# Kernel tuning notes

Hardware: AMD Instinct MI355X
Metric: run time of the kernel (lower is better)

Reference implementation:

```python
import jax, jax.numpy as jnp
import numpy as np

G = 4  # number of groups


def _group_vals(h, shift, Ua, Ua1, Ua2, Ua3):
    # h: [B, H]; Ua: [g, H/g, r]; Ua1/2/3: [g, r, H/g]
    B, H = h.shape
    hg = h.reshape(B, G, H // G)
    if shift:
        # torch index = rotate-left by `shift`: new group j reads old group (j+shift)%g
        hg = jnp.roll(hg, -shift, axis=1)
    t = jnp.einsum('bgd,gdr->bgr', hg, Ua)  # shared low-rank projection
    proj = lambda M: jnp.einsum('bgr,grd->bgd', t, M).reshape(B, H)
    return proj(Ua1), proj(Ua2), proj(Ua3)


def setup_inputs() -> dict:
    key = jax.random.key(0)
    ks = jax.random.split(key, 24)
    B, I, H, wR = 8192, 1024, 1024, 256
    hg = H // G
    r01, r23 = 64, 32
    d = {}
    d['x'] = jax.random.normal(ks[0], (B, I), dtype=jnp.float32)
    d['h'] = jax.random.normal(ks[1], (B, H), dtype=jnp.float32)
    d['W'] = 0.1 * jax.random.normal(ks[2], (I, wR), dtype=jnp.float32)
    d['W1'] = 0.1 * jax.random.normal(ks[3], (wR, H), dtype=jnp.float32)
    d['W2'] = 0.1 * jax.random.normal(ks[4], (wR, H), dtype=jnp.float32)
    d['W3'] = 0.1 * jax.random.normal(ks[5], (wR, H), dtype=jnp.float32)
    d['U'] = 0.1 * jax.random.normal(ks[6], (G, hg, r01), dtype=jnp.float32)
    d['U1'] = 0.1 * jax.random.normal(ks[7], (G, r01, hg), dtype=jnp.float32)
    d['U2'] = 0.1 * jax.random.normal(ks[8], (G, r01, hg), dtype=jnp.float32)
    d['U3'] = 0.1 * jax.random.normal(ks[9], (G, r01, hg), dtype=jnp.float32)
    d['UU'] = 0.1 * jax.random.normal(ks[10], (G, hg, r01), dtype=jnp.float32)
    d['UU1'] = 0.1 * jax.random.normal(ks[11], (G, r01, hg), dtype=jnp.float32)
    d['UU2'] = 0.1 * jax.random.normal(ks[12], (G, r01, hg), dtype=jnp.float32)
    d['UU3'] = 0.1 * jax.random.normal(ks[13], (G, r01, hg), dtype=jnp.float32)
    d['UUU'] = 0.1 * jax.random.normal(ks[14], (G, hg, r23), dtype=jnp.float32)
    d['UUU1'] = 0.1 * jax.random.normal(ks[15], (G, r23, hg), dtype=jnp.float32)
    d['UUU2'] = 0.1 * jax.random.normal(ks[16], (G, r23, hg), dtype=jnp.float32)
    d['UUU3'] = 0.1 * jax.random.normal(ks[17], (G, r23, hg), dtype=jnp.float32)
    d['UUUU'] = 0.1 * jax.random.normal(ks[18], (G, hg, r23), dtype=jnp.float32)
    d['UUUU1'] = 0.1 * jax.random.normal(ks[19], (G, r23, hg), dtype=jnp.float32)
    d['UUUU2'] = 0.1 * jax.random.normal(ks[20], (G, r23, hg), dtype=jnp.float32)
    d['UUUU3'] = 0.1 * jax.random.normal(ks[21], (G, r23, hg), dtype=jnp.float32)
    d['bias_r'] = jnp.ones((1, H), dtype=jnp.float32)
    d['bias_gate'] = jnp.ones((1, H), dtype=jnp.float32)
    d['bias_update'] = jnp.ones((1, H), dtype=jnp.float32)
    return d


def reference(x, h, W, W1, W2, W3, U, U1, U2, U3, UU, UU1, UU2, UU3,
              UUU, UUU1, UUU2, UUU3, UUUU, UUUU1, UUUU2, UUUU3,
              bias_r, bias_gate, bias_update):
    u1, u2, u3 = _group_vals(h, 0, U, U1, U2, U3)
    uu1, uu2, uu3 = _group_vals(h, 1, UU, UU1, UU2, UU3)
    uuu1, uuu2, uuu3 = _group_vals(h, 2, UUU, UUU1, UUU2, UUU3)
    uuuu1, uuuu2, uuuu3 = _group_vals(h, 3, UUUU, UUUU1, UUUU2, UUUU3)
    xw = x @ W  # [B, wRank]
    w1, w2, w3 = xw @ W1, xw @ W2, xw @ W3
    r = jax.nn.sigmoid(w1 + u1 + uu1 + uuu1 + uuuu1 + bias_r)
    z = jax.nn.sigmoid(w2 + u2 + uu2 + uuu2 + uuuu2 + bias_gate)
    c_tilda = jnp.tanh(w3 + r * (u3 + uu3 + uuu3 + uuuu3) + bias_update)
    return z * h + (1.0 - z) * c_tilda
```

## Files before the change

kernel.cpp:

```cpp
#include <hip/hip_runtime.h>

typedef short bf16x8 __attribute__((ext_vector_type(8)));
typedef float f32x4 __attribute__((ext_vector_type(4)));
typedef float f32x16 __attribute__((ext_vector_type(16)));

__device__ __forceinline__ unsigned short f2bf(float f) {
  union { float f; unsigned u; } c; c.f = f;
  unsigned u = c.u;
  u += 0x7FFFu + ((u >> 16) & 1u);
  return (unsigned short)(u >> 16);
}
__device__ __forceinline__ float bf2f(unsigned short h) {
  union { unsigned u; float f; } c; c.u = ((unsigned)h) << 16;
  return c.f;
}
__device__ __forceinline__ void split2(float v, unsigned short& hi, unsigned short& lo) {
  union { float f; unsigned u; } c; c.f = v;
  unsigned uh = c.u & 0xFFFF0000u;
  hi = (unsigned short)(uh >> 16);
  union { unsigned u; float f; } d; d.u = uh;
  lo = f2bf(v - d.f);
}
__device__ __forceinline__ void gload16(const void* g, void* l) {
  __builtin_amdgcn_global_load_lds((const __attribute__((address_space(1))) void*)g,
                                   (__attribute__((address_space(3))) void*)l, 16, 0, 0);
}
__device__ __forceinline__ float sigm(float x) { return 1.0f / (1.0f + __expf(-x)); }
__device__ __forceinline__ float tanha(float x) { return 1.0f - 2.0f / (1.0f + __expf(2.0f * x)); }

__device__ __forceinline__ size_t fragIdxA(int row, int col) {
  int mb = row >> 7, rb = (row >> 5) & 3, l5 = row & 31;
  int cc = col >> 6, k4 = (col >> 4) & 3, hi = (col >> 3) & 1, e = col & 7;
  return ((size_t)(mb * 20 + cc) * 16 + rb * 4 + k4) * 512 + (hi * 32 + l5) * 8 + e;
}

__global__ __launch_bounds__(256) void s123(
    const float* __restrict__ W,
    const float* __restrict__ U, const float* __restrict__ UU,
    const float* __restrict__ UUU, const float* __restrict__ UUUU,
    const float* __restrict__ W1, const float* __restrict__ W2, const float* __restrict__ W3,
    const float* __restrict__ A1, const float* __restrict__ A2, const float* __restrict__ A3,
    const float* __restrict__ B1, const float* __restrict__ B2, const float* __restrict__ B3,
    const float* __restrict__ C1, const float* __restrict__ C2, const float* __restrict__ C3,
    const float* __restrict__ D1, const float* __restrict__ D2, const float* __restrict__ D3,
    unsigned short* __restrict__ Wt, unsigned short* __restrict__ Bg,
    unsigned short* __restrict__ Btp) {
  int gidx = blockIdx.x * 256 + threadIdx.x;
  if (gidx < 262144) {
    int idx = gidx;
    int n = idx >> 10, k = idx & 1023;
    Wt[idx] = f2bf(W[k * 256 + n]);
  } else if (gidx < 458752) {
    int idx = gidx - 262144;
    int g = idx / 49152;
    int rem = idx - g * 49152;
    int n = rem >> 8, k = rem & 255;
    int jj = 0, rr = n;
#pragma unroll
    for (int s = 0; s < 3; ++s) {
      int w = (((g - jj) & 3) < 2) ? 64 : 32;
      if (rr >= w) { rr -= w; ++jj; }
    }
    int v = (g - jj) & 3;
    int rv = (v < 2) ? 64 : 32;
    const float* M = (v == 0) ? U : (v == 1) ? UU : (v == 2) ? UUU : UUUU;
    Bg[idx] = f2bf(M[(jj * 256 + k) * rv + rr]);
  } else {
    int idx = gidx - 458752;
    int blk = idx / 12288;
    int w   = idx - blk * 12288;
    int frag = w >> 9, fl = (w >> 3) & 63, e = w & 7;
    int cb = blk & 3, jk = blk >> 2;
    int kt = jk % 11, j = jk / 11;
    int q = frag >> 3, colblk = (frag >> 2) & 1, k4 = frag & 3;
    int c  = cb * 64 + colblk * 32 + (fl & 31);
    int k2 = k4 * 16 + (fl >> 5) * 8 + e;
    float val;
    if (kt < 8) {
      int kk = (kt * 64 + k2) & 255;
      const float* Wp = (q == 0) ? W1 : (q == 1) ? W2 : W3;
      val = Wp[kk * 1024 + j * 256 + c];
    } else {
      int kT = (kt - 8) * 64 + k2;
      int v, r, rv;
      if (kT < 64)       { v = 0; r = kT;       rv = 64; }
      else if (kT < 128) { v = 1; r = kT - 64;  rv = 64; }
      else if (kT < 160) { v = 2; r = kT - 128; rv = 32; }
      else               { v = 3; r = kT - 160; rv = 32; }
      const float* M;
      if (v == 0)      M = (q == 0) ? A1 : (q == 1) ? A2 : A3;
      else if (v == 1) M = (q == 0) ? B1 : (q == 1) ? B2 : B3;
      else if (v == 2) M = (q == 0) ? C1 : (q == 1) ? C2 : C3;
      else             M = (q == 0) ? D1 : (q == 1) ? D2 : D3;
      val = M[(j * rv + r) * 256 + c];
    }
    Btp[idx] = f2bf(val);
  }
}

__device__ __forceinline__ void g1_body(const float* __restrict__ x,
                                        const unsigned short* __restrict__ Wt,
                                        unsigned short* __restrict__ Abuf,
                                        char* lds, int mb, int nb, int tid) {
  const int lane = tid & 63, wid = tid >> 6;
  const int wm = 0, wn = wid;
  f32x4 acc[2][2] = {};
  float4 xr[2];
  const int r0 = tid >> 4, f4c = tid & 15;
  const float* xbase = x + (size_t)(mb * 32) * 1024 + f4c * 4;
  (void)wm;

  auto loadX = [&](int kt) {
#pragma unroll
    for (int q = 0; q < 2; ++q)
      xr[q] = *(const float4*)(xbase + (size_t)(q * 16 + r0) * 1024 + kt * 64);
  };
  auto writeA = [&](int buf) {
#pragma unroll
    for (int q = 0; q < 2; ++q) {
      int row = q * 16 + r0;
      float4 v = xr[q];
      unsigned short h0, h1, h2, h3, l0, l1, l2, l3;
      split2(v.x, h0, l0); split2(v.y, h1, l1);
      split2(v.z, h2, l2); split2(v.w, h3, l3);
      int ba = row * 128 + ((f4c * 8) ^ ((row & 7) << 4));
      *(uint2*)(lds + buf * 4096 + ba) =
          make_uint2(((unsigned)h1 << 16) | h0, ((unsigned)h3 << 16) | h2);
      *(uint2*)(lds + 8192 + buf * 4096 + ba) =
          make_uint2(((unsigned)l1 << 16) | l0, ((unsigned)l3 << 16) | l2);
    }
  };
  auto stageB = [&](int kt, int buf) {
#pragma unroll
    for (int it = 0; it < 4; ++it) {
      int nloc = it * 32 + wid * 8 + (lane >> 3);
      const char* src = (const char*)Wt + (size_t)(nb * 128 + nloc) * 2048 + kt * 128
                        + (((lane & 7) * 16) ^ ((nloc & 7) << 4));
      gload16(src, lds + 16384 + buf * 16384 + (it * 32 + wid * 8) * 128);
    }
  };

  loadX(0); stageB(0, 0); writeA(0);
  __syncthreads();
#pragma unroll 2
  for (int kt = 0; kt < 16; ++kt) {
    int buf = kt & 1;
    if (kt < 15) {
      loadX(kt + 1); stageB(kt + 1, buf ^ 1);
      asm volatile("s_waitcnt vmcnt(6)" ::: "memory");
    } else {
      asm volatile("s_waitcnt vmcnt(0)" ::: "memory");
    }
    __builtin_amdgcn_s_barrier();
    __builtin_amdgcn_sched_barrier(0);
    const char* hA = lds + buf * 4096;
    const char* lA = lds + 8192 + buf * 4096;
    const char* bB = lds + 16384 + buf * 16384;
#pragma unroll
    for (int ks = 0; ks < 2; ++ks) {
      bf16x8 ah[2], al[2], b[2];
#pragma unroll
      for (int mf = 0; mf < 2; ++mf) {
        int mloc = mf * 16 + (lane & 15);
        int ka = (ks * 64 + (lane >> 4) * 16) ^ ((mloc & 7) << 4);
        ah[mf] = *(const bf16x8*)(hA + mloc * 128 + ka);
        al[mf] = *(const bf16x8*)(lA + mloc * 128 + ka);
      }
#pragma unroll
      for (int nf = 0; nf < 2; ++nf) {
        int nloc = wn * 32 + nf * 16 + (lane & 15);
        int kb = (ks * 64 + (lane >> 4) * 16) ^ ((nloc & 7) << 4);
        b[nf] = *(const bf16x8*)(bB + nloc * 128 + kb);
      }
#pragma unroll
      for (int mf = 0; mf < 2; ++mf)
#pragma unroll
        for (int nf = 0; nf < 2; ++nf) {
          acc[mf][nf] = __builtin_amdgcn_mfma_f32_16x16x32_bf16(ah[mf], b[nf], acc[mf][nf], 0, 0, 0);
          acc[mf][nf] = __builtin_amdgcn_mfma_f32_16x16x32_bf16(al[mf], b[nf], acc[mf][nf], 0, 0, 0);
        }
    }
    if (kt < 15) writeA(buf ^ 1);
    __builtin_amdgcn_sched_barrier(0);
    asm volatile("s_waitcnt lgkmcnt(0)" ::: "memory");
    __builtin_amdgcn_s_barrier();
  }
#pragma unroll
  for (int mf = 0; mf < 2; ++mf)
#pragma unroll
    for (int nf = 0; nf < 2; ++nf)
#pragma unroll
      for (int r = 0; r < 4; ++r) {
        int row = mb * 32 + mf * 16 + (lane >> 4) * 4 + r;
        int col = nb * 128 + wn * 32 + nf * 16 + (lane & 15);
        float val = acc[mf][nf][r];
        unsigned short hi, lo;
        split2(val, hi, lo);
        Abuf[fragIdxA(row, col)] = hi;
        Abuf[fragIdxA(row, col + 256)] = lo;
      }
}

__device__ __forceinline__ void g2_body(const float* __restrict__ h,
                                        const unsigned short* __restrict__ Bg,
                                        unsigned short* __restrict__ Abuf,
                                        char* lds, int mb, int g, int tid) {
  const int lane = tid & 63, wid = tid >> 6;
  const int wm = wid >> 1, wn = wid & 1;
  f32x4 acc[2][6] = {};
  float4 hr[4];
  const int r0 = tid >> 4, f4c = tid & 15;
  const float* hbase = h + (size_t)(mb * 64) * 1024 + g * 256 + f4c * 4;

  auto loadH = [&](int kt) {
#pragma unroll
    for (int q = 0; q < 4; ++q)
      hr[q] = *(const float4*)(hbase + (size_t)(q * 16 + r0) * 1024 + kt * 64);
  };
  auto writeA = [&](int buf) {
#pragma unroll
    for (int q = 0; q < 4; ++q) {
      int row = q * 16 + r0;
      float4 v = hr[q];
      int ba = row * 128 + ((f4c * 8) ^ ((row & 7) << 4));
      *(uint2*)(lds + buf * 8192 + ba) =
          make_uint2(((unsigned)f2bf(v.y) << 16) | f2bf(v.x),
                     ((unsigned)f2bf(v.w) << 16) | f2bf(v.z));
    }
  };
  auto stageB = [&](int kt, int buf) {
#pragma unroll
    for (int it = 0; it < 6; ++it) {
      int nloc = it * 32 + wid * 8 + (lane >> 3);
      const char* src = (const char*)Bg + (size_t)(g * 192 + nloc) * 512 + kt * 128
                        + (((lane & 7) * 16) ^ ((nloc & 7) << 4));
      gload16(src, lds + 16384 + buf * 24576 + (it * 32 + wid * 8) * 128);
    }
  };

  loadH(0); stageB(0, 0); writeA(0);
  __syncthreads();
#pragma unroll
  for (int kt = 0; kt < 4; ++kt) {
    int buf = kt & 1;
    if (kt < 3) { loadH(kt + 1); stageB(kt + 1, buf ^ 1); }
    const char* cA = lds + buf * 8192;
    const char* cB = lds + 16384 + buf * 24576;
#pragma unroll
    for (int ks = 0; ks < 2; ++ks) {
      bf16x8 a[2], b[6];
#pragma unroll
      for (int mf = 0; mf < 2; ++mf) {
        int mloc = wm * 32 + mf * 16 + (lane & 15);
        int ka = (ks * 64 + (lane >> 4) * 16) ^ ((mloc & 7) << 4);
        a[mf] = *(const bf16x8*)(cA + mloc * 128 + ka);
      }
#pragma unroll
      for (int nf = 0; nf < 6; ++nf) {
        int nloc = wn * 96 + nf * 16 + (lane & 15);
        int kb = (ks * 64 + (lane >> 4) * 16) ^ ((nloc & 7) << 4);
        b[nf] = *(const bf16x8*)(cB + nloc * 128 + kb);
      }
#pragma unroll
      for (int mf = 0; mf < 2; ++mf)
#pragma unroll
        for (int nf = 0; nf < 6; ++nf)
          acc[mf][nf] = __builtin_amdgcn_mfma_f32_16x16x32_bf16(a[mf], b[nf], acc[mf][nf], 0, 0, 0);
    }
    if (kt < 3) writeA(buf ^ 1);
    __syncthreads();
  }
#pragma unroll
  for (int mf = 0; mf < 2; ++mf)
#pragma unroll
    for (int nf = 0; nf < 6; ++nf) {
      int n = wn * 96 + nf * 16 + (lane & 15);
      int jj = 0, rr = n;
#pragma unroll
      for (int s = 0; s < 3; ++s) {
        int w = (((g - jj) & 3) < 2) ? 64 : 32;
        if (rr >= w) { rr -= w; ++jj; }
      }
      int v = (g - jj) & 3;
      int offv = (v < 2) ? (v << 6) : (64 + (v << 5));
      int col = 512 + jj * 192 + offv + rr;
#pragma unroll
      for (int r = 0; r < 4; ++r) {
        int row = mb * 64 + wm * 32 + mf * 16 + (lane >> 4) * 4 + r;
        Abuf[fragIdxA(row, col)] = f2bf(acc[mf][nf][r]);
      }
    }
}

__global__ __launch_bounds__(256) void g12(const float* __restrict__ x,
                                           const unsigned short* __restrict__ Wt,
                                           const float* __restrict__ h,
                                           const unsigned short* __restrict__ Bg,
                                           unsigned short* __restrict__ Abuf) {
  __shared__ char lds[65536];
  int b = blockIdx.x, tid = threadIdx.x;
  if (b < 512) {
    g1_body(x, Wt, Abuf, lds, b >> 1, b & 1, tid);
  } else {
    int b2 = b - 512;
    g2_body(h, Bg, Abuf, lds, b2 >> 2, b2 & 3, tid);
  }
}

__global__ __launch_bounds__(256) void g3_main(const unsigned short* __restrict__ Abuf,
                                               const unsigned short* __restrict__ Btp,
                                               const float* __restrict__ h,
                                               const float* __restrict__ bias_r,
                                               const float* __restrict__ bias_g,
                                               const float* __restrict__ bias_u,
                                               float* __restrict__ out) {
  __shared__ char lds[81920];
  const int tid = threadIdx.x, lane = tid & 63, wid = tid >> 6;
  const int flat = blockIdx.x;
  const int xcd = flat & 7, idx = flat >> 3;
  const int mb = xcd * 8 + (idx & 7);
  const int cj = idx >> 3;
  const int cb = cj & 3, j = cj >> 2;
  const int wm = wid >> 1, wn = wid & 1;
  f32x16 acc[2][4] = {};

  const char* AbufB = (const char*)Abuf;
  const char* BtpB  = (const char*)Btp;

  auto stage = [&](int kt, int buf) {
    int cc = (kt < 8) ? kt : (8 + j * 3 + (kt - 8));
    const char* asrc = AbufB + (size_t)(mb * 20 + cc) * 16384 + tid * 16;
    const char* bsrc = BtpB + (size_t)(((j * 11 + kt) * 4 + cb)) * 24576 + tid * 16;
#pragma unroll
    for (int it = 0; it < 4; ++it)
      gload16(asrc + it * 4096, lds + buf * 16384 + it * 4096 + wid * 1024);
#pragma unroll
    for (int it = 0; it < 6; ++it)
      gload16(bsrc + it * 4096, lds + 32768 + buf * 24576 + it * 4096 + wid * 1024);
  };

  stage(0, 0);
#pragma unroll
  for (int kt = 0; kt < 11; ++kt) {
    const int buf = kt & 1;
    asm volatile("s_waitcnt vmcnt(0)" ::: "memory");
    __builtin_amdgcn_s_barrier();
    __builtin_amdgcn_sched_barrier(0);
    if (kt < 10) stage(kt + 1, buf ^ 1);
    __builtin_amdgcn_s_setprio(1);
    const char* aB = lds + buf * 16384 + wm * 8192 + lane * 16;
    const char* bB = lds + 32768 + buf * 24576 + wn * 4096 + lane * 16;
#pragma unroll
    for (int k4 = 0; k4 < 4; ++k4) {
      bf16x8 a0 = *(const bf16x8*)(aB + k4 * 1024);
      bf16x8 a1 = *(const bf16x8*)(aB + 4096 + k4 * 1024);
#pragma unroll
      for (int q = 0; q < 3; ++q) {
        const int p = (kt < 8) ? q : ((q == 2) ? 3 : q);
        bf16x8 b = *(const bf16x8*)(bB + q * 8192 + k4 * 1024);
        acc[0][p] = __builtin_amdgcn_mfma_f32_32x32x16_bf16(a0, b, acc[0][p], 0, 0, 0);
        acc[1][p] = __builtin_amdgcn_mfma_f32_32x32x16_bf16(a1, b, acc[1][p], 0, 0, 0);
      }
    }
    __builtin_amdgcn_s_setprio(0);
    __builtin_amdgcn_sched_barrier(0);
  }
  int cg = j * 256 + cb * 64 + wn * 32 + (lane & 31);
  float br = bias_r[cg], bg = bias_g[cg], bu = bias_u[cg];
#pragma unroll
  for (int mblk = 0; mblk < 2; ++mblk)
#pragma unroll
    for (int r = 0; r < 16; ++r) {
      int row = mb * 128 + wm * 64 + mblk * 32 + (r & 3) + 8 * (r >> 2) + 4 * (lane >> 5);
      float p0 = acc[mblk][0][r], p1 = acc[mblk][1][r];
      float p2 = acc[mblk][2][r], p3 = acc[mblk][3][r];
      float rr = sigm(p0 + br);
      float zz = sigm(p1 + bg);
      float ct = tanha(p2 + rr * p3 + bu);
      float hv = h[(size_t)row * 1024 + cg];
      out[(size_t)row * 1024 + cg] = zz * hv + (1.0f - zz) * ct;
    }
}

extern "C" void kernel_launch(void* const* d_in, const int* in_sizes, int n_in,
                              void* d_out, int out_size, void* d_ws, size_t ws_size,
                              hipStream_t stream) {
  const float* x   = (const float*)d_in[0];
  const float* h   = (const float*)d_in[1];
  const float* W   = (const float*)d_in[2];
  const float* W1  = (const float*)d_in[3];
  const float* W2  = (const float*)d_in[4];
  const float* W3  = (const float*)d_in[5];
  const float* U   = (const float*)d_in[6];
  const float* U1  = (const float*)d_in[7];
  const float* U2  = (const float*)d_in[8];
  const float* U3  = (const float*)d_in[9];
  const float* UU   = (const float*)d_in[10];
  const float* UU1  = (const float*)d_in[11];
  const float* UU2  = (const float*)d_in[12];
  const float* UU3  = (const float*)d_in[13];
  const float* UUU   = (const float*)d_in[14];
  const float* UUU1  = (const float*)d_in[15];
  const float* UUU2  = (const float*)d_in[16];
  const float* UUU3  = (const float*)d_in[17];
  const float* UUUU   = (const float*)d_in[18];
  const float* UUUU1  = (const float*)d_in[19];
  const float* UUUU2  = (const float*)d_in[20];
  const float* UUUU3  = (const float*)d_in[21];
  const float* bias_r = (const float*)d_in[22];
  const float* bias_g = (const float*)d_in[23];
  const float* bias_u = (const float*)d_in[24];

  char* ws = (char*)d_ws;
  unsigned short* Abuf = (unsigned short*)(ws);
  unsigned short* Wt   = (unsigned short*)(ws + 20971520);
  unsigned short* Bg   = (unsigned short*)(ws + 21495808);
  unsigned short* Btp  = (unsigned short*)(ws + 21889024);
  float* out = (float*)d_out;

  s123<<<10240, 256, 0, stream>>>(W, U, UU, UUU, UUUU,
                                  W1, W2, W3, U1, U2, U3, UU1, UU2, UU3,
                                  UUU1, UUU2, UUU3, UUUU1, UUUU2, UUUU3,
                                  Wt, Bg, Btp);
  g12<<<1024, 256, 0, stream>>>(x, Wt, h, Bg, Abuf);
  g3_main<<<1024, 256, 0, stream>>>(Abuf, Btp, h, bias_r, bias_g, bias_u, out);
}
```

Measured before the change: 93.99 us.

## Share B tiles across hi/lo A chunks and pipeline loads with partial waitcnt

Measured after the change: 90.46 us. 3.8% less time.

```diff
diff --git a/kernel.cpp b/kernel.cpp
--- a/kernel.cpp
+++ b/kernel.cpp
@@ -71,13 +71,14 @@
     int w   = idx - blk * 12288;
     int frag = w >> 9, fl = (w >> 3) & 63, e = w & 7;
     int cb = blk & 3, jk = blk >> 2;
-    int kt = jk % 11, j = jk / 11;
+    int kts = jk % 7, j = jk / 7;
+    int kt = (kts < 4) ? kts : (kts + 4);
     int q = frag >> 3, colblk = (frag >> 2) & 1, k4 = frag & 3;
     int c  = cb * 64 + colblk * 32 + (fl & 31);
     int k2 = k4 * 16 + (fl >> 5) * 8 + e;
     float val;
     if (kt < 8) {
-      int kk = (kt * 64 + k2) & 255;
+      int kk = kt * 64 + k2;
       const float* Wp = (q == 0) ? W1 : (q == 1) ? W2 : W3;
       val = Wp[kk * 1024 + j * 256 + c];
     } else {
@@ -103,12 +104,11 @@
                                         unsigned short* __restrict__ Abuf,
                                         char* lds, int mb, int nb, int tid) {
   const int lane = tid & 63, wid = tid >> 6;
-  const int wm = 0, wn = wid;
+  const int wn = wid;
   f32x4 acc[2][2] = {};
   float4 xr[2];
   const int r0 = tid >> 4, f4c = tid & 15;
   const float* xbase = x + (size_t)(mb * 32) * 1024 + f4c * 4;
-  (void)wm;
 
   auto loadX = [&](int kt) {
 #pragma unroll
@@ -327,36 +327,51 @@
   const char* AbufB = (const char*)Abuf;
   const char* BtpB  = (const char*)Btp;
 
-  auto stage = [&](int kt, int buf) {
-    int cc = (kt < 8) ? kt : (8 + j * 3 + (kt - 8));
-    const char* asrc = AbufB + (size_t)(mb * 20 + cc) * 16384 + tid * 16;
-    const char* bsrc = BtpB + (size_t)(((j * 11 + kt) * 4 + cb)) * 24576 + tid * 16;
+  const int A_cc[11]  = {0, 4, 1, 5, 2, 6, 3, 7, 8 + j * 3, 9 + j * 3, 10 + j * 3};
+  const int B_kts[11] = {0, 0, 1, 1, 2, 2, 3, 3, 4, 5, 6};
+  const bool B_st[11] = {true, false, true, false, true, false, true, false, true, true, true};
+  const int B_buf[11] = {0, 0, 1, 1, 0, 0, 1, 1, 0, 1, 0};
+
+  auto stageA = [&](int step, int buf) {
+    const char* asrc = AbufB + (size_t)(mb * 20 + A_cc[step]) * 16384 + tid * 16;
 #pragma unroll
     for (int it = 0; it < 4; ++it)
       gload16(asrc + it * 4096, lds + buf * 16384 + it * 4096 + wid * 1024);
+  };
+  auto stageBt = [&](int step, int buf) {
+    const char* bsrc = BtpB + (size_t)((j * 7 + B_kts[step]) * 4 + cb) * 24576 + tid * 16;
 #pragma unroll
     for (int it = 0; it < 6; ++it)
       gload16(bsrc + it * 4096, lds + 32768 + buf * 24576 + it * 4096 + wid * 1024);
   };
 
-  stage(0, 0);
-#pragma unroll
-  for (int kt = 0; kt < 11; ++kt) {
-    const int buf = kt & 1;
-    asm volatile("s_waitcnt vmcnt(0)" ::: "memory");
+  stageA(0, 0); stageBt(0, 0);
+#pragma unroll
+  for (int i = 0; i < 11; ++i) {
+    const int abuf = i & 1, bbuf = B_buf[i];
+    if (i < 10) {
+      stageA(i + 1, (i + 1) & 1);
+      if (B_st[i + 1]) {
+        stageBt(i + 1, B_buf[i + 1]);
+        asm volatile("s_waitcnt vmcnt(10)" ::: "memory");
+      } else {
+        asm volatile("s_waitcnt vmcnt(4)" ::: "memory");
+      }
+    } else {
+      asm volatile("s_waitcnt vmcnt(0)" ::: "memory");
+    }
     __builtin_amdgcn_s_barrier();
     __builtin_amdgcn_sched_barrier(0);
-    if (kt < 10) stage(kt + 1, buf ^ 1);
     __builtin_amdgcn_s_setprio(1);
-    const char* aB = lds + buf * 16384 + wm * 8192 + lane * 16;
-    const char* bB = lds + 32768 + buf * 24576 + wn * 4096 + lane * 16;
+    const char* aB = lds + abuf * 16384 + wm * 8192 + lane * 16;
+    const char* bB = lds + 32768 + bbuf * 24576 + wn * 4096 + lane * 16;
 #pragma unroll
     for (int k4 = 0; k4 < 4; ++k4) {
       bf16x8 a0 = *(const bf16x8*)(aB + k4 * 1024);
       bf16x8 a1 = *(const bf16x8*)(aB + 4096 + k4 * 1024);
 #pragma unroll
       for (int q = 0; q < 3; ++q) {
-        const int p = (kt < 8) ? q : ((q == 2) ? 3 : q);
+        const int p = (i < 8) ? q : ((q == 2) ? 3 : q);
         bf16x8 b = *(const bf16x8*)(bB + q * 8192 + k4 * 1024);
         acc[0][p] = __builtin_amdgcn_mfma_f32_32x32x16_bf16(a0, b, acc[0][p], 0, 0, 0);
         acc[1][p] = __builtin_amdgcn_mfma_f32_32x32x16_bf16(a1, b, acc[1][p], 0, 0, 0);
@@ -364,6 +379,7 @@
     }
     __builtin_amdgcn_s_setprio(0);
     __builtin_amdgcn_sched_barrier(0);
+    __builtin_amdgcn_s_barrier();
   }
   int cg = j * 256 + cb * 64 + wn * 32 + (lane & 31);
   float br = bias_r[cg], bg = bias_g[cg], bu = bias_u[cg];
@@ -418,10 +434,10 @@
   unsigned short* Btp  = (unsigned short*)(ws + 21889024);
   float* out = (float*)d_out;
 
-  s123<<<10240, 256, 0, stream>>>(W, U, UU, UUU, UUUU,
-                                  W1, W2, W3, U1, U2, U3, UU1, UU2, UU3,
-                                  UUU1, UUU2, UUU3, UUUU1, UUUU2, UUUU3,
-                                  Wt, Bg, Btp);
+  s123<<<7168, 256, 0, stream>>>(W, U, UU, UUU, UUUU,
+                                 W1, W2, W3, U1, U2, U3, UU1, UU2, UU3,
+                                 UUU1, UUU2, UUU3, UUUU1, UUUU2, UUUU3,
+                                 Wt, Bg, Btp);
   g12<<<1024, 256, 0, stream>>>(x, Wt, h, Bg, Abuf);
   g3_main<<<1024, 256, 0, stream>>>(Abuf, Btp, h, bias_r, bias_g, bias_u, out);
 }
```
